# Kernel tuning notes

Measured on AMD Instinct MI355X. Metric: run time of the kernel, lower is better.

## Reference

```python
import jax, jax.numpy as jnp
from jax import lax
import numpy as np

L, B, D, H = 256, 128, 512, 512


def setup_inputs() -> dict:
    rng = np.random.default_rng(0)
    # random projective-ish dependency trees: node 0 is root, head[i] < i
    heads = np.full((B, L), -1, dtype=np.int64)
    for i in range(1, L):
        heads[:, i] = rng.integers(0, i, size=B)
    # bottom-up traversal order (children have larger index than parent)
    indexes = np.tile(np.arange(L - 1, -1, -1, dtype=np.int32)[:, None], (1, B))  # [L,B]
    # cm_full[b,p,j] = 1 if j is a child of p in tree b
    cm_full = (heads[:, None, :] == np.arange(L)[None, :, None]).astype(np.float32)  # [B,L,L]
    child_mask = cm_full[:, ::-1, :].transpose(1, 0, 2).copy()  # [L,B,L] aligned with indexes
    # top-down order: root first (ascending index works since head[i] < i)
    td_node = np.tile(np.arange(L, dtype=np.int32)[:, None], (1, B))  # [L,B]
    td_parent_idx = np.maximum(heads.T, 0).astype(np.int32)  # [L,B]
    td_parent_valid = (heads.T >= 0).astype(np.float32)  # [L,B], 0 at root
    root_index = np.zeros(B, dtype=np.int32)

    key = jax.random.key(0)
    ks = jax.random.split(key, 7)
    sx = 1.0 / np.sqrt(D)
    sh = 1.0 / np.sqrt(H)
    return {
        "emb": jax.random.normal(ks[0], (L, B, D), jnp.float32),
        "indexes": jnp.asarray(indexes),
        "child_mask": jnp.asarray(child_mask),
        "td_node": jnp.asarray(td_node),
        "td_parent_idx": jnp.asarray(td_parent_idx),
        "td_parent_valid": jnp.asarray(td_parent_valid),
        "root_index": jnp.asarray(root_index),
        "dt_Wx": jax.random.normal(ks[1], (D, 3 * H), jnp.float32) * sx,
        "dt_Uh": jax.random.normal(ks[2], (H, 3 * H), jnp.float32) * sh,
        "dt_b": jnp.zeros((3 * H,), jnp.float32),
        "td_Wx": jax.random.normal(ks[3], (D, 3 * H), jnp.float32) * sx,
        "td_Uh": jax.random.normal(ks[4], (H, 3 * H), jnp.float32) * sh,
        "td_b": jnp.zeros((3 * H,), jnp.float32),
    }


def _gru_cell(x, h, Wx, Uh, b):
    # standard GRU: gates laid out as [r, z, n]
    xg = x @ Wx + b
    hg = h @ Uh
    xr, xz, xn = jnp.split(xg, 3, axis=-1)
    hr, hz, hn = jnp.split(hg, 3, axis=-1)
    r = jax.nn.sigmoid(xr + hr)
    z = jax.nn.sigmoid(xz + hz)
    n = jnp.tanh(xn + r * hn)
    return (1.0 - z) * n + z * h


def reference(emb, indexes, child_mask, td_node, td_parent_idx, td_parent_valid,
              root_index, dt_Wx, dt_Uh, dt_b, td_Wx, td_Uh, td_b):
    Ld, Bd, Dd = emb.shape
    Hd = dt_Uh.shape[0]
    barange = jnp.arange(Bd)

    # ---- bottom-up (DT) pass: h_prev = sum of children hiddens ----
    x_dt = jnp.take_along_axis(emb, indexes[:, :, None], axis=0)  # [L,B,D]

    def dt_step(Hs, xs):
        x, node, cmask = xs                      # [B,D], [B], [B,L]
        h = jnp.einsum('bl,blh->bh', cmask, Hs)  # sum over children
        hn = _gru_cell(x, h, dt_Wx, dt_Uh, dt_b)
        return Hs.at[barange, node].set(hn), None

    Hdt, _ = lax.scan(dt_step, jnp.zeros((Bd, Ld, Hd), emb.dtype),
                      (x_dt, indexes, child_mask))

    # ---- top-down (TD) pass: h_prev = parent hidden (zeros at root) ----
    x_td = jnp.take_along_axis(emb, td_node[:, :, None], axis=0)  # [L,B,D]

    def td_step(Hs, xs):
        x, node, pidx, pvalid = xs
        h = Hs[barange, pidx] * pvalid[:, None]
        hn = _gru_cell(x, h, td_Wx, td_Uh, td_b)
        return Hs.at[barange, node].set(hn), None

    Htd, _ = lax.scan(td_step, jnp.zeros((Bd, Ld, Hd), emb.dtype),
                      (x_td, td_node, td_parent_idx, td_parent_valid))

    outputs = jnp.concatenate([Hdt, Htd], axis=-1)  # [B,L,2H] (batch-first as original)
    root_h = jnp.concatenate([Hdt[barange, root_index], Htd[barange, root_index]], axis=-1)
    output_t = root_h[None]  # [1,B,2H]
    return outputs, output_t
```

## Files before the change

### kernel.cpp

```cpp
#include <hip/hip_runtime.h>
#include <hip/hip_cooperative_groups.h>


#define NL 256
#define NB 128
#define NH 512
#define NG (NB * NL)
#define WLDS 98304

typedef short short8 __attribute__((ext_vector_type(8)));
typedef float f32x4 __attribute__((ext_vector_type(4)));

__device__ __forceinline__ float bf2f(unsigned short u) {
  union { unsigned int i; float f; } c; c.i = ((unsigned int)u) << 16; return c.f;
}
__device__ __forceinline__ unsigned short f2bf(float f) {
  union { float f; unsigned int i; } c; c.f = f;
  return (unsigned short)((c.i + 0x7FFFu + ((c.i >> 16) & 1u)) >> 16);
}
__device__ __forceinline__ short8 pk_bf16(f32x4 a, f32x4 b) {
  union { unsigned int u[4]; short8 s; } r;
  asm("v_cvt_pk_bf16_f32 %0, %1, %2" : "=v"(r.u[0]) : "v"(a[0]), "v"(a[1]));
  asm("v_cvt_pk_bf16_f32 %0, %1, %2" : "=v"(r.u[1]) : "v"(a[2]), "v"(a[3]));
  asm("v_cvt_pk_bf16_f32 %0, %1, %2" : "=v"(r.u[2]) : "v"(b[0]), "v"(b[1]));
  asm("v_cvt_pk_bf16_f32 %0, %1, %2" : "=v"(r.u[3]) : "v"(b[2]), "v"(b[3]));
  return r.s;
}
__device__ __forceinline__ void atom_pk_bf16(unsigned short* p, unsigned int ud) {
  asm volatile("global_atomic_pk_add_bf16 %0, %1, off" :: "v"((void*)p), "v"(ud) : "memory");
}

__global__ void prep_wt4(const float* __restrict__ w0, const float* __restrict__ w1,
                         const float* __restrict__ w2, const float* __restrict__ w3,
                         unsigned short* __restrict__ wt) {
  __shared__ float t[32][33];
  const float* w = blockIdx.z == 0 ? w0 : blockIdx.z == 1 ? w1 : blockIdx.z == 2 ? w2 : w3;
  unsigned short* dst = wt + (size_t)blockIdx.z * 1536 * 512;
  int n0 = blockIdx.x * 32, k0 = blockIdx.y * 32;
  int tx = threadIdx.x & 31, ty = threadIdx.x >> 5;
  #pragma unroll
  for (int i = 0; i < 4; ++i)
    t[ty + 8 * i][tx] = w[(size_t)(k0 + ty + 8 * i) * 1536 + n0 + tx];
  __syncthreads();
  #pragma unroll
  for (int i = 0; i < 4; ++i)
    dst[(size_t)(n0 + ty + 8 * i) * 512 + k0 + tx] = f2bf(t[tx][ty + 8 * i]);
}

__global__ void prep_sched(const int* __restrict__ td_pidx,
                           const float* __restrict__ td_pval,
                           int* __restrict__ sched, int* __restrict__ meta,
                           int* __restrict__ gidx, int* __restrict__ pslot) {
  __shared__ unsigned char dep[NB][NL];
  __shared__ unsigned short cnb[NB][256];
  __shared__ int cnt[256];
  __shared__ int off[257];
  __shared__ int dmax_s;
  const int tid = threadIdx.x;
  for (int j = tid; j < NB * 256; j += 256) ((unsigned short*)cnb)[j] = 0;
  if (tid == 0) dmax_s = 0;
  __syncthreads();
  if (tid < NB) {
    int b = tid, lmax = 0;
    for (int i = 0; i < NL; ++i) {
      float pv = td_pval[i * NB + b];
      int pi = td_pidx[i * NB + b];
      int d = (pv != 0.f) ? (int)dep[b][pi] + 1 : 0;
      dep[b][i] = (unsigned char)d;
      cnb[b][d]++;
      lmax = max(lmax, d);
    }
    atomicMax(&dmax_s, lmax);
  }
  __syncthreads();
  {
    int s = 0;
    for (int b = 0; b < NB; ++b) s += cnb[b][tid];
    cnt[tid] = s;
  }
  __syncthreads();
  if (tid == 0) {
    int s = 0;
    for (int d = 0; d < 256; ++d) { off[d] = s; s += cnt[d]; }
    off[256] = s;
  }
  __syncthreads();
  {
    int run = off[tid];
    for (int b = 0; b < NB; ++b) {
      int t = cnb[b][tid];
      cnb[b][tid] = (unsigned short)run;
      run += t;
    }
  }
  __syncthreads();
  if (tid < NB) {
    int b = tid;
    for (int i = 0; i < NL; ++i) {
      float pv = td_pval[i * NB + b];
      int pi = td_pidx[i * NB + b];
      int d = dep[b][i];
      int g = cnb[b][d]++;
      sched[g] = (b << 8) | i;
      gidx[b * NL + i] = g;
      pslot[g] = (pv != 0.f) ? gidx[b * NL + pi] : -1;
    }
  }
  if (tid == 0) meta[0] = dmax_s;
  __syncthreads();
  meta[1 + tid] = off[tid];
  meta[257 + tid] = cnt[tid];
}

__global__ void prep_xc(const float* __restrict__ emb, const int* __restrict__ sched,
                        unsigned short* __restrict__ Xc) {
  int g = blockIdx.x * 4 + (threadIdx.x >> 6);
  int lane = threadIdx.x & 63;
  int e = sched[g];
  int b = e >> 8, node = e & 255;
  const float* src = emb + ((size_t)node * NB + b) * 512 + lane * 8;
  f32x4 v0 = *(const f32x4*)src;
  f32x4 v1 = *(const f32x4*)(src + 4);
  *(short8*)(Xc + (size_t)g * 512 + lane * 8) = pk_bf16(v0, v1);
}

__launch_bounds__(512, 2)
__global__ void tree_gru(const float* __restrict__ dt_b,
                         const float* __restrict__ td_b,
                         const unsigned short* __restrict__ wt,
                         const unsigned short* __restrict__ Xc,
                         unsigned short* __restrict__ Hdt,
                         unsigned short* __restrict__ Htd,
                         const unsigned short* __restrict__ zrow,
                         const int* __restrict__ sched,
                         const int* __restrict__ meta,
                         const int* __restrict__ pslot,
                         const int* __restrict__ root_index,
                         float* __restrict__ out) {
  extern __shared__ unsigned char lds[];
  const int tid = threadIdx.x;
  const int bi  = blockIdx.x;
  const int pass = bi >> 7;
  const int rep  = (bi >> 5) & 3;
  const int cg   = bi & 31;
  const int w  = tid >> 6, l = tid & 63;
  const int lm = l & 15, kg = l >> 4;
  const int col = cg * 16 + lm;

  for (int idx = tid; idx < 6144; idx += 512) {
    int k8  = idx & 63;
    int n   = (idx >> 6) & 15;
    int g   = (idx >> 10) % 3;
    int mat = idx / 3072;
    const unsigned short* src = wt + (size_t)(pass * 2 + mat) * (1536 * 512)
                                   + (size_t)(g * 512 + cg * 16 + n) * 512 + k8 * 8;
    short8 v = *(const short8*)src;
    int off = ((mat * 3 + g) * 16 + n) * 1024 + ((k8 * 16) ^ ((n & 7) << 4));
    *(short8*)(lds + off) = v;
  }
  unsigned char* Xb = lds + WLDS;
  unsigned char* Hb = lds + WLDS + 16384;
  __syncthreads();

  const float* bias = pass ? td_b : dt_b;
  const float br = bias[col], bz = bias[NH + col], bn = bias[2 * NH + col];
  const int base_wr = (0 * 16 + lm) * 1024;
  const int base_wz = (1 * 16 + lm) * 1024;
  const int base_wn = (2 * 16 + lm) * 1024;
  const int base_ur = (3 * 16 + lm) * 1024;
  const int base_uz = (4 * 16 + lm) * 1024;
  const int base_un = (5 * 16 + lm) * 1024;
  const int wswz = (lm & 7) << 4;

  const int srow = tid >> 3, sslot = tid & 7;
  const int dsw = ((sslot ^ (srow & 7)) << 4);

  cooperative_groups::grid_group grid = cooperative_groups::this_grid();
  const int Dmax = meta[0];

  for (int p = 0; p <= Dmax; ++p) {
    const int d = pass ? p : (Dmax - p);
    const int off_d = meta[1 + d];
    const int cnt_d = meta[257 + d];
    const int T = (cnt_d + 127) >> 7;
    for (int t = rep; t < T; t += 4) {
      const int g0 = off_d + t * 128;
      const int rows = min(128, cnt_d - t * 128);
      const unsigned short *sx[2], *sh[2];
      #pragma unroll
      for (int i = 0; i < 2; ++i) {
        int r = min(i * 64 + srow, rows - 1);
        int gg = g0 + r;
        sx[i] = Xc + (size_t)gg * 512 + sslot * 8;
        if (pass == 0) {
          sh[i] = Hdt + (size_t)gg * 512 + sslot * 8;
        } else {
          int ps = pslot[gg];
          sh[i] = (ps >= 0 ? Htd + (size_t)ps * 512 : zrow) + sslot * 8;
        }
      }
      short8 rx0 = *(const short8*)sx[0], rx1 = *(const short8*)sx[1];
      short8 rh0 = *(const short8*)sh[0], rh1 = *(const short8*)sh[1];
      f32x4 aR = {0,0,0,0}, aZ = {0,0,0,0}, aXN = {0,0,0,0}, aHN = {0,0,0,0};
      for (int c = 0; c < 8; ++c) {
        __syncthreads();
        *(short8*)(Xb + (srow)      * 128 + dsw) = rx0;
        *(short8*)(Xb + (64 + srow) * 128 + dsw) = rx1;
        *(short8*)(Hb + (srow)      * 128 + dsw) = rh0;
        *(short8*)(Hb + (64 + srow) * 128 + dsw) = rh1;
        if (c < 7) {
          rx0 = *(const short8*)(sx[0] + (c + 1) * 64);
          rx1 = *(const short8*)(sx[1] + (c + 1) * 64);
          rh0 = *(const short8*)(sh[0] + (c + 1) * 64);
          rh1 = *(const short8*)(sh[1] + (c + 1) * 64);
        }
        __syncthreads();
        #pragma unroll
        for (int ks = 0; ks < 2; ++ks) {
          const int so = (((ks << 2) | kg) ^ (lm & 7)) << 4;
          const int arow = w * 16 + lm;
          short8 ax = *(const short8*)(Xb + arow * 128 + so);
          short8 ah = *(const short8*)(Hb + arow * 128 + so);
          const int kb = (c * 128 + ks * 64 + kg * 16) ^ wswz;
          short8 bwr = *(const short8*)(lds + base_wr + kb);
          short8 bwz = *(const short8*)(lds + base_wz + kb);
          short8 bwn = *(const short8*)(lds + base_wn + kb);
          short8 bur = *(const short8*)(lds + base_ur + kb);
          short8 buz = *(const short8*)(lds + base_uz + kb);
          short8 bun = *(const short8*)(lds + base_un + kb);
          aR  = __builtin_amdgcn_mfma_f32_16x16x32_bf16(ax, bwr, aR, 0, 0, 0);
          aZ  = __builtin_amdgcn_mfma_f32_16x16x32_bf16(ax, bwz, aZ, 0, 0, 0);
          aXN = __builtin_amdgcn_mfma_f32_16x16x32_bf16(ax, bwn, aXN, 0, 0, 0);
          aR  = __builtin_amdgcn_mfma_f32_16x16x32_bf16(ah, bur, aR, 0, 0, 0);
          aZ  = __builtin_amdgcn_mfma_f32_16x16x32_bf16(ah, buz, aZ, 0, 0, 0);
          aHN = __builtin_amdgcn_mfma_f32_16x16x32_bf16(ah, bun, aHN, 0, 0, 0);
        }
      }
      #pragma unroll
      for (int q = 0; q < 4; ++q) {
        const int r = w * 16 + kg * 4 + q;
        if (r >= rows) continue;
        const int g = g0 + r;
        const int e = sched[g];
        const int bO = e >> 8, node = e & 255;
        const int ps = pslot[g];
        float hprev;
        if (pass == 0) hprev = bf2f(Hdt[(size_t)g * 512 + col]);
        else           hprev = (ps >= 0) ? bf2f(Htd[(size_t)ps * 512 + col]) : 0.f;
        float rr = 1.f / (1.f + __expf(-(aR[q] + br)));
        float zz = 1.f / (1.f + __expf(-(aZ[q] + bz)));
        float e2 = __expf(2.f * (aXN[q] + bn + rr * aHN[q]));
        float nn = (e2 - 1.f) / (e2 + 1.f);
        float h = (1.f - zz) * nn + zz * hprev;
        __builtin_nontemporal_store(h, &out[((size_t)bO * NL + node) * 1024 + pass * 512 + col]);
        float ho = __shfl_xor(h, 1);
        if (!(lm & 1)) {
          unsigned int ud;
          asm("v_cvt_pk_bf16_f32 %0, %1, %2" : "=v"(ud) : "v"(h), "v"(ho));
          if (pass == 0) {
            if (ps >= 0) atom_pk_bf16(Hdt + (size_t)ps * 512 + col, ud);
          } else {
            *(unsigned int*)(Htd + (size_t)g * 512 + col) = ud;
          }
        }
      }
    }
    grid.sync();
  }

  if (bi < NB) {
    int b = bi, root = root_index[b];
    for (int c = tid; c < 1024; c += 512)
      out[(size_t)NB * NL * 1024 + (size_t)b * 1024 + c] =
          out[((size_t)b * NL + root) * 1024 + c];
  }
}

extern "C" void kernel_launch(void* const* d_in, const int* in_sizes, int n_in,
                              void* d_out, int out_size, void* d_ws, size_t ws_size,
                              hipStream_t stream) {
  (void)in_sizes; (void)n_in; (void)out_size; (void)ws_size;
  const float* emb      = (const float*)d_in[0];
  const int*   td_pidx  = (const int*)d_in[4];
  const float* td_pval  = (const float*)d_in[5];
  const int*   root_idx = (const int*)d_in[6];
  const float* dt_Wx    = (const float*)d_in[7];
  const float* dt_Uh    = (const float*)d_in[8];
  const float* dt_b     = (const float*)d_in[9];
  const float* td_Wx    = (const float*)d_in[10];
  const float* td_Uh    = (const float*)d_in[11];
  const float* td_b     = (const float*)d_in[12];
  float* out = (float*)d_out;

  unsigned short* wt   = (unsigned short*)d_ws;
  unsigned short* Xc   = wt + (size_t)4 * 1536 * 512;
  unsigned short* Hdt  = Xc + (size_t)NG * NH;
  unsigned short* zrow = Hdt + (size_t)NG * NH;
  unsigned short* Htd  = zrow + NH;
  int* sched = (int*)(Htd + (size_t)NG * NH);
  int* meta  = sched + NG;
  int* gidx  = meta + 520;
  int* pslot = gidx + NG;

  (void)hipMemsetAsync(Hdt, 0, ((size_t)NG * NH + NH) * 2, stream);
  prep_wt4<<<dim3(48, 16, 4), dim3(256), 0, stream>>>(dt_Wx, dt_Uh, td_Wx, td_Uh, wt);
  prep_sched<<<dim3(1), dim3(256), 0, stream>>>(td_pidx, td_pval, sched, meta, gidx, pslot);
  prep_xc<<<dim3(NG / 4), dim3(256), 0, stream>>>(emb, sched, Xc);

  (void)hipFuncSetAttribute((const void*)tree_gru,
                            hipFuncAttributeMaxDynamicSharedMemorySize, 131072);

  void* args[] = {
    (void*)&dt_b, (void*)&td_b, (void*)&wt, (void*)&Xc, (void*)&Hdt, (void*)&Htd,
    (void*)&zrow, (void*)&sched, (void*)&meta, (void*)&pslot, (void*)&root_idx, (void*)&out
  };
  (void)hipLaunchCooperativeKernel((const void*)tree_gru, dim3(256), dim3(512),
                                   args, 131072u, stream);
}
```

Baseline: 1.635 ms.

## Retile tree GRU to 256x64 tiles with 32x32 MFMA and deferred output write

The tree GRU kernel moves from 128-row by 16-column tiles with resident LDS weights to 256-row by 64-column tiles. It uses 32x32x16 MFMAs, and weights are streamed per K-chunk alongside the activations, starting at a staggered K offset per column group. The fp32 output scatter and root copy leave the recurrent loop. Hidden states are stored as bf16 in a new buffer and expanded by a separate finalize kernel, and h_prev is read back from LDS instead of global memory. The aim is more MFMA work per LDS load and less global traffic inside the serialized level loop. The cost is reloading weights from global/L2 on every tile, fewer tiles per level to spread across blocks, and an extra bf16 round trip for outputs.

```diff
diff --git a/kernel.cpp b/kernel.cpp
--- a/kernel.cpp
+++ b/kernel.cpp
@@ -6,10 +6,10 @@
 #define NB 128
 #define NH 512
 #define NG (NB * NL)
-#define WLDS 98304
 
 typedef short short8 __attribute__((ext_vector_type(8)));
 typedef float f32x4 __attribute__((ext_vector_type(4)));
+typedef float f32x16 __attribute__((ext_vector_type(16)));
 
 __device__ __forceinline__ float bf2f(unsigned short u) {
   union { unsigned int i; float f; } c; c.i = ((unsigned int)u) << 16; return c.f;
@@ -130,50 +130,44 @@
                          const unsigned short* __restrict__ wt,
                          const unsigned short* __restrict__ Xc,
                          unsigned short* __restrict__ Hdt,
+                         unsigned short* __restrict__ Hfd,
                          unsigned short* __restrict__ Htd,
                          const unsigned short* __restrict__ zrow,
-                         const int* __restrict__ sched,
                          const int* __restrict__ meta,
-                         const int* __restrict__ pslot,
-                         const int* __restrict__ root_index,
-                         float* __restrict__ out) {
+                         const int* __restrict__ pslot) {
   extern __shared__ unsigned char lds[];
+  unsigned char* Axb = lds;
+  unsigned char* Ahb = lds + 32768;
+  unsigned char* Bwb = lds + 65536;
   const int tid = threadIdx.x;
   const int bi  = blockIdx.x;
   const int pass = bi >> 7;
-  const int rep  = (bi >> 5) & 3;
-  const int cg   = bi & 31;
-  const int w  = tid >> 6, l = tid & 63;
-  const int lm = l & 15, kg = l >> 4;
-  const int col = cg * 16 + lm;
-
-  for (int idx = tid; idx < 6144; idx += 512) {
-    int k8  = idx & 63;
-    int n   = (idx >> 6) & 15;
-    int g   = (idx >> 10) % 3;
-    int mat = idx / 3072;
-    const unsigned short* src = wt + (size_t)(pass * 2 + mat) * (1536 * 512)
-                                   + (size_t)(g * 512 + cg * 16 + n) * 512 + k8 * 8;
-    short8 v = *(const short8*)src;
-    int off = ((mat * 3 + g) * 16 + n) * 1024 + ((k8 * 16) ^ ((n & 7) << 4));
-    *(short8*)(lds + off) = v;
-  }
-  unsigned char* Xb = lds + WLDS;
-  unsigned char* Hb = lds + WLDS + 16384;
-  __syncthreads();
-
+  const int rp   = (bi >> 3) & 15;
+  const int cg   = bi & 7;
+  const int w = tid >> 6, l = tid & 63;
+  const int wr = w >> 1, wc = w & 1;
+  const int l31 = l & 31, lh = l >> 5;
+  const int col = cg * 64 + wc * 32 + l31;
   const float* bias = pass ? td_b : dt_b;
   const float br = bias[col], bz = bias[NH + col], bn = bias[2 * NH + col];
-  const int base_wr = (0 * 16 + lm) * 1024;
-  const int base_wz = (1 * 16 + lm) * 1024;
-  const int base_wn = (2 * 16 + lm) * 1024;
-  const int base_ur = (3 * 16 + lm) * 1024;
-  const int base_uz = (4 * 16 + lm) * 1024;
-  const int base_un = (5 * 16 + lm) * 1024;
-  const int wswz = (lm & 7) << 4;
-
-  const int srow = tid >> 3, sslot = tid & 7;
-  const int dsw = ((sslot ^ (srow & 7)) << 4);
+
+  const unsigned short* bsrc[6];
+  int bdst[6];
+  #pragma unroll
+  for (int i = 0; i < 6; ++i) {
+    int j = tid + 512 * i;
+    int nrow = j >> 3, slot = j & 7;
+    int s = nrow >> 6, n = nrow & 63;
+    int side = (s >= 3) ? 1 : 0;
+    int gate = s - side * 3;
+    bsrc[i] = wt + (size_t)(pass * 2 + side) * (1536 * 512)
+                 + (size_t)(gate * 512 + cg * 64 + n) * 512 + slot * 8;
+    bdst[i] = nrow * 128 + ((slot * 16) ^ ((nrow & 7) << 4));
+  }
+  const int srow = tid >> 1;
+  const int sh64 = (tid & 1) * 64;
+  const int sdswz = (srow & 7) << 4;
+  const int rsw = (l31 & 7) << 4;
 
   cooperative_groups::grid_group grid = cooperative_groups::this_grid();
   const int Dmax = meta[0];
@@ -182,97 +176,153 @@
     const int d = pass ? p : (Dmax - p);
     const int off_d = meta[1 + d];
     const int cnt_d = meta[257 + d];
-    const int T = (cnt_d + 127) >> 7;
-    for (int t = rep; t < T; t += 4) {
-      const int g0 = off_d + t * 128;
-      const int rows = min(128, cnt_d - t * 128);
-      const unsigned short *sx[2], *sh[2];
-      #pragma unroll
-      for (int i = 0; i < 2; ++i) {
-        int r = min(i * 64 + srow, rows - 1);
-        int gg = g0 + r;
-        sx[i] = Xc + (size_t)gg * 512 + sslot * 8;
-        if (pass == 0) {
-          sh[i] = Hdt + (size_t)gg * 512 + sslot * 8;
-        } else {
-          int ps = pslot[gg];
-          sh[i] = (ps >= 0 ? Htd + (size_t)ps * 512 : zrow) + sslot * 8;
+    const int T = (cnt_d + 255) >> 8;
+    for (int t = rp; t < T; t += 16) {
+      const int g0 = off_d + t * 256;
+      const int rows = min(256, cnt_d - t * 256);
+      const int gg = g0 + min(srow, rows - 1);
+      const unsigned short* sxp = Xc + (size_t)gg * 512 + (tid & 1) * 32;
+      const unsigned short* shp;
+      if (pass == 0) {
+        shp = Hdt + (size_t)gg * 512 + (tid & 1) * 32;
+      } else {
+        int ps = pslot[gg];
+        shp = (ps >= 0 ? Htd + (size_t)ps * 512 : zrow) + (tid & 1) * 32;
+      }
+      short8 rx[4], rh[4], rb[6];
+      const int c0 = (cg + 1) & 7;
+      #pragma unroll
+      for (int jj = 0; jj < 4; ++jj) {
+        rx[jj] = *(const short8*)(sxp + c0 * 64 + jj * 8);
+        rh[jj] = *(const short8*)(shp + c0 * 64 + jj * 8);
+      }
+      #pragma unroll
+      for (int i = 0; i < 6; ++i) rb[i] = *(const short8*)(bsrc[i] + c0 * 64);
+
+      f32x16 aR[2], aZ[2], aXN[2], aHN[2];
+      #pragma unroll
+      for (int rf = 0; rf < 2; ++rf) {
+        #pragma unroll
+        for (int e = 0; e < 16; ++e) { aR[rf][e] = 0.f; aZ[rf][e] = 0.f; aXN[rf][e] = 0.f; aHN[rf][e] = 0.f; }
+      }
+
+      for (int ci = 0; ci < 8; ++ci) {
+        const int kb0 = ((cg + 1 + ci) & 7) * 0;
+        (void)kb0;
+        __syncthreads();
+        #pragma unroll
+        for (int jj = 0; jj < 4; ++jj) {
+          *(short8*)(Axb + srow * 128 + ((sh64 + jj * 16) ^ sdswz)) = rx[jj];
+          *(short8*)(Ahb + srow * 128 + ((sh64 + jj * 16) ^ sdswz)) = rh[jj];
         }
-      }
-      short8 rx0 = *(const short8*)sx[0], rx1 = *(const short8*)sx[1];
-      short8 rh0 = *(const short8*)sh[0], rh1 = *(const short8*)sh[1];
-      f32x4 aR = {0,0,0,0}, aZ = {0,0,0,0}, aXN = {0,0,0,0}, aHN = {0,0,0,0};
-      for (int c = 0; c < 8; ++c) {
-        __syncthreads();
-        *(short8*)(Xb + (srow)      * 128 + dsw) = rx0;
-        *(short8*)(Xb + (64 + srow) * 128 + dsw) = rx1;
-        *(short8*)(Hb + (srow)      * 128 + dsw) = rh0;
-        *(short8*)(Hb + (64 + srow) * 128 + dsw) = rh1;
-        if (c < 7) {
-          rx0 = *(const short8*)(sx[0] + (c + 1) * 64);
-          rx1 = *(const short8*)(sx[1] + (c + 1) * 64);
-          rh0 = *(const short8*)(sh[0] + (c + 1) * 64);
-          rh1 = *(const short8*)(sh[1] + (c + 1) * 64);
+        #pragma unroll
+        for (int i = 0; i < 6; ++i) *(short8*)(Bwb + bdst[i]) = rb[i];
+        if (ci < 7) {
+          const int cn = (cg + 2 + ci) & 7;
+          #pragma unroll
+          for (int jj = 0; jj < 4; ++jj) {
+            rx[jj] = *(const short8*)(sxp + cn * 64 + jj * 8);
+            rh[jj] = *(const short8*)(shp + cn * 64 + jj * 8);
+          }
+          #pragma unroll
+          for (int i = 0; i < 6; ++i) rb[i] = *(const short8*)(bsrc[i] + cn * 64);
         }
         __syncthreads();
         #pragma unroll
-        for (int ks = 0; ks < 2; ++ks) {
-          const int so = (((ks << 2) | kg) ^ (lm & 7)) << 4;
-          const int arow = w * 16 + lm;
-          short8 ax = *(const short8*)(Xb + arow * 128 + so);
-          short8 ah = *(const short8*)(Hb + arow * 128 + so);
-          const int kb = (c * 128 + ks * 64 + kg * 16) ^ wswz;
-          short8 bwr = *(const short8*)(lds + base_wr + kb);
-          short8 bwz = *(const short8*)(lds + base_wz + kb);
-          short8 bwn = *(const short8*)(lds + base_wn + kb);
-          short8 bur = *(const short8*)(lds + base_ur + kb);
-          short8 buz = *(const short8*)(lds + base_uz + kb);
-          short8 bun = *(const short8*)(lds + base_un + kb);
-          aR  = __builtin_amdgcn_mfma_f32_16x16x32_bf16(ax, bwr, aR, 0, 0, 0);
-          aZ  = __builtin_amdgcn_mfma_f32_16x16x32_bf16(ax, bwz, aZ, 0, 0, 0);
-          aXN = __builtin_amdgcn_mfma_f32_16x16x32_bf16(ax, bwn, aXN, 0, 0, 0);
-          aR  = __builtin_amdgcn_mfma_f32_16x16x32_bf16(ah, bur, aR, 0, 0, 0);
-          aZ  = __builtin_amdgcn_mfma_f32_16x16x32_bf16(ah, buz, aZ, 0, 0, 0);
-          aHN = __builtin_amdgcn_mfma_f32_16x16x32_bf16(ah, bun, aHN, 0, 0, 0);
+        for (int ks = 0; ks < 4; ++ks) {
+          const int kb = (ks * 32 + lh * 16) ^ rsw;
+          short8 ax0 = *(const short8*)(Axb + (wr * 64 + l31) * 128 + kb);
+          short8 ax1 = *(const short8*)(Axb + (wr * 64 + 32 + l31) * 128 + kb);
+          short8 ah0 = *(const short8*)(Ahb + (wr * 64 + l31) * 128 + kb);
+          short8 ah1 = *(const short8*)(Ahb + (wr * 64 + 32 + l31) * 128 + kb);
+          short8 b0 = *(const short8*)(Bwb + (0 * 64 + wc * 32 + l31) * 128 + kb);
+          short8 b1 = *(const short8*)(Bwb + (1 * 64 + wc * 32 + l31) * 128 + kb);
+          short8 b2 = *(const short8*)(Bwb + (2 * 64 + wc * 32 + l31) * 128 + kb);
+          short8 b3 = *(const short8*)(Bwb + (3 * 64 + wc * 32 + l31) * 128 + kb);
+          short8 b4 = *(const short8*)(Bwb + (4 * 64 + wc * 32 + l31) * 128 + kb);
+          short8 b5 = *(const short8*)(Bwb + (5 * 64 + wc * 32 + l31) * 128 + kb);
+          aR[0]  = __builtin_amdgcn_mfma_f32_32x32x16_bf16(ax0, b0, aR[0], 0, 0, 0);
+          aR[1]  = __builtin_amdgcn_mfma_f32_32x32x16_bf16(ax1, b0, aR[1], 0, 0, 0);
+          aZ[0]  = __builtin_amdgcn_mfma_f32_32x32x16_bf16(ax0, b1, aZ[0], 0, 0, 0);
+          aZ[1]  = __builtin_amdgcn_mfma_f32_32x32x16_bf16(ax1, b1, aZ[1], 0, 0, 0);
+          aXN[0] = __builtin_amdgcn_mfma_f32_32x32x16_bf16(ax0, b2, aXN[0], 0, 0, 0);
+          aXN[1] = __builtin_amdgcn_mfma_f32_32x32x16_bf16(ax1, b2, aXN[1], 0, 0, 0);
+          aR[0]  = __builtin_amdgcn_mfma_f32_32x32x16_bf16(ah0, b3, aR[0], 0, 0, 0);
+          aR[1]  = __builtin_amdgcn_mfma_f32_32x32x16_bf16(ah1, b3, aR[1], 0, 0, 0);
+          aZ[0]  = __builtin_amdgcn_mfma_f32_32x32x16_bf16(ah0, b4, aZ[0], 0, 0, 0);
+          aZ[1]  = __builtin_amdgcn_mfma_f32_32x32x16_bf16(ah1, b4, aZ[1], 0, 0, 0);
+          aHN[0] = __builtin_amdgcn_mfma_f32_32x32x16_bf16(ah0, b5, aHN[0], 0, 0, 0);
+          aHN[1] = __builtin_amdgcn_mfma_f32_32x32x16_bf16(ah1, b5, aHN[1], 0, 0, 0);
         }
       }
       #pragma unroll
-      for (int q = 0; q < 4; ++q) {
-        const int r = w * 16 + kg * 4 + q;
-        if (r >= rows) continue;
-        const int g = g0 + r;
-        const int e = sched[g];
-        const int bO = e >> 8, node = e & 255;
-        const int ps = pslot[g];
-        float hprev;
-        if (pass == 0) hprev = bf2f(Hdt[(size_t)g * 512 + col]);
-        else           hprev = (ps >= 0) ? bf2f(Htd[(size_t)ps * 512 + col]) : 0.f;
-        float rr = 1.f / (1.f + __expf(-(aR[q] + br)));
-        float zz = 1.f / (1.f + __expf(-(aZ[q] + bz)));
-        float e2 = __expf(2.f * (aXN[q] + bn + rr * aHN[q]));
-        float nn = (e2 - 1.f) / (e2 + 1.f);
-        float h = (1.f - zz) * nn + zz * hprev;
-        __builtin_nontemporal_store(h, &out[((size_t)bO * NL + node) * 1024 + pass * 512 + col]);
-        float ho = __shfl_xor(h, 1);
-        if (!(lm & 1)) {
-          unsigned int ud;
-          asm("v_cvt_pk_bf16_f32 %0, %1, %2" : "=v"(ud) : "v"(h), "v"(ho));
-          if (pass == 0) {
-            if (ps >= 0) atom_pk_bf16(Hdt + (size_t)ps * 512 + col, ud);
-          } else {
-            *(unsigned int*)(Htd + (size_t)g * 512 + col) = ud;
+      for (int rf = 0; rf < 2; ++rf) {
+        #pragma unroll
+        for (int reg = 0; reg < 16; ++reg) {
+          const int row = wr * 64 + rf * 32 + (reg & 3) + 8 * (reg >> 2) + 4 * lh;
+          if (row < rows) {
+            const int g = g0 + row;
+            const int hb = row * 128 + ((2 * (wc * 32 + l31)) ^ ((row & 7) << 4));
+            const float hprev = bf2f(*(const unsigned short*)(Ahb + hb));
+            float rr = 1.f / (1.f + __expf(-(aR[rf][reg] + br)));
+            float zz = 1.f / (1.f + __expf(-(aZ[rf][reg] + bz)));
+            float e2 = __expf(2.f * (aXN[rf][reg] + bn + rr * aHN[rf][reg]));
+            float nn = (e2 - 1.f) / (e2 + 1.f);
+            float h = (1.f - zz) * nn + zz * hprev;
+            float ho = __shfl_xor(h, 1);
+            if (!(l & 1)) {
+              unsigned int ud;
+              asm("v_cvt_pk_bf16_f32 %0, %1, %2" : "=v"(ud) : "v"(h), "v"(ho));
+              if (pass == 0) {
+                *(unsigned int*)(Hfd + (size_t)g * 512 + col) = ud;
+                int ps = pslot[g];
+                if (ps >= 0) atom_pk_bf16(Hdt + (size_t)ps * 512 + col, ud);
+              } else {
+                *(unsigned int*)(Htd + (size_t)g * 512 + col) = ud;
+              }
+            }
           }
         }
       }
     }
     grid.sync();
   }
-
-  if (bi < NB) {
-    int b = bi, root = root_index[b];
-    for (int c = tid; c < 1024; c += 512)
-      out[(size_t)NB * NL * 1024 + (size_t)b * 1024 + c] =
-          out[((size_t)b * NL + root) * 1024 + c];
+}
+
+__global__ void finalize(const unsigned short* __restrict__ Hfd,
+                         const unsigned short* __restrict__ Htd,
+                         const int* __restrict__ sched,
+                         const int* __restrict__ root_index,
+                         float* __restrict__ out) {
+  const int g = blockIdx.x * 16 + (threadIdx.x >> 4);
+  const int part = threadIdx.x & 15;
+  const int e = sched[g];
+  const int b = e >> 8, node = e & 255;
+  float* dst = out + ((size_t)b * NL + node) * 1024;
+  const bool isroot = (node == root_index[b]);
+  float* dst2 = out + (size_t)NB * NL * 1024 + (size_t)b * 1024;
+  const unsigned short* s1 = Hfd + (size_t)g * 512 + part * 32;
+  const unsigned short* s2 = Htd + (size_t)g * 512 + part * 32;
+  #pragma unroll
+  for (int half = 0; half < 2; ++half) {
+    const unsigned short* s = half ? s2 : s1;
+    const int o = half * 512 + part * 32;
+    #pragma unroll
+    for (int j = 0; j < 4; ++j) {
+      short8 v = *(const short8*)(s + j * 8);
+      f32x4 lo, hi;
+      #pragma unroll
+      for (int q = 0; q < 4; ++q) {
+        lo[q] = bf2f((unsigned short)v[q]);
+        hi[q] = bf2f((unsigned short)v[4 + q]);
+      }
+      __builtin_nontemporal_store(lo, (f32x4*)(dst + o + j * 8));
+      __builtin_nontemporal_store(hi, (f32x4*)(dst + o + j * 8 + 4));
+      if (isroot) {
+        *(f32x4*)(dst2 + o + j * 8) = lo;
+        *(f32x4*)(dst2 + o + j * 8 + 4) = hi;
+      }
+    }
   }
 }
 
@@ -296,7 +346,8 @@
   unsigned short* Xc   = wt + (size_t)4 * 1536 * 512;
   unsigned short* Hdt  = Xc + (size_t)NG * NH;
   unsigned short* zrow = Hdt + (size_t)NG * NH;
-  unsigned short* Htd  = zrow + NH;
+  unsigned short* Hfd  = zrow + NH;
+  unsigned short* Htd  = Hfd + (size_t)NG * NH;
   int* sched = (int*)(Htd + (size_t)NG * NH);
   int* meta  = sched + NG;
   int* gidx  = meta + 520;
@@ -308,12 +359,13 @@
   prep_xc<<<dim3(NG / 4), dim3(256), 0, stream>>>(emb, sched, Xc);
 
   (void)hipFuncSetAttribute((const void*)tree_gru,
-                            hipFuncAttributeMaxDynamicSharedMemorySize, 131072);
+                            hipFuncAttributeMaxDynamicSharedMemorySize, 114688);
 
   void* args[] = {
-    (void*)&dt_b, (void*)&td_b, (void*)&wt, (void*)&Xc, (void*)&Hdt, (void*)&Htd,
-    (void*)&zrow, (void*)&sched, (void*)&meta, (void*)&pslot, (void*)&root_idx, (void*)&out
+    (void*)&dt_b, (void*)&td_b, (void*)&wt, (void*)&Xc, (void*)&Hdt, (void*)&Hfd,
+    (void*)&Htd, (void*)&zrow, (void*)&meta, (void*)&pslot
   };
   (void)hipLaunchCooperativeKernel((const void*)tree_gru, dim3(256), dim3(512),
-                                   args, 131072u, stream);
-}
+                                   args, 114688u, stream);
+  finalize<<<dim3(NG / 16), dim3(256), 0, stream>>>(Hfd, Htd, sched, root_idx, out);
+}
```

After: 2.561 ms. 1.57x slower.

## Replace grid-wide barriers with per-level dependency counters and deferred output writes

Applied to the files above, without the earlier changes.

Swaps the cooperative grid.sync after every depth level for per-level atomic completion counters. Each block spin-waits only on the level it depends on, and blocks with no tiles at a level skip it, so the DT and TD passes can proceed independently. Final hidden states are now kept in bf16 workspace (a new Hfd buffer for DT) and expanded to fp32 output in one coalesced epilogue that also writes the root rows. hprev is read from the LDS tile instead of global memory, the K-chunk start is staggered per column group, and the block-to-work mapping is changed. The cost is spin-wait polling, extra atomics and fences, an extra workspace buffer, and a larger memset.

```diff
diff --git a/kernel.cpp b/kernel.cpp
--- a/kernel.cpp
+++ b/kernel.cpp
@@ -1,12 +1,10 @@
 #include <hip/hip_runtime.h>
-#include <hip/hip_cooperative_groups.h>
 
 
 #define NL 256
 #define NB 128
 #define NH 512
 #define NG (NB * NL)
-#define WLDS 98304
 
 typedef short short8 __attribute__((ext_vector_type(8)));
 typedef float f32x4 __attribute__((ext_vector_type(4)));
@@ -28,6 +26,15 @@
 }
 __device__ __forceinline__ void atom_pk_bf16(unsigned short* p, unsigned int ud) {
   asm volatile("global_atomic_pk_add_bf16 %0, %1, off" :: "v"((void*)p), "v"(ud) : "memory");
+}
+
+__device__ __forceinline__ void level_wait(unsigned int* c, unsigned int target) {
+  if (threadIdx.x == 0) {
+    while (__hip_atomic_load(c, __ATOMIC_RELAXED, __HIP_MEMORY_SCOPE_AGENT) < target)
+      __builtin_amdgcn_s_sleep(8);
+  }
+  __syncthreads();
+  __builtin_amdgcn_fence(__ATOMIC_ACQUIRE, "agent");
 }
 
 __global__ void prep_wt4(const float* __restrict__ w0, const float* __restrict__ w1,
@@ -131,18 +138,20 @@
                          const unsigned short* __restrict__ Xc,
                          unsigned short* __restrict__ Hdt,
                          unsigned short* __restrict__ Htd,
+                         unsigned short* __restrict__ Hfd,
                          const unsigned short* __restrict__ zrow,
-                         const int* __restrict__ sched,
                          const int* __restrict__ meta,
                          const int* __restrict__ pslot,
+                         unsigned int* __restrict__ ctr,
+                         const int* __restrict__ sched,
                          const int* __restrict__ root_index,
                          float* __restrict__ out) {
   extern __shared__ unsigned char lds[];
   const int tid = threadIdx.x;
   const int bi  = blockIdx.x;
-  const int pass = bi >> 7;
-  const int rep  = (bi >> 5) & 3;
-  const int cg   = bi & 31;
+  const int cg   = bi >> 3;
+  const int pass = (bi >> 2) & 1;
+  const int rep  = bi & 3;
   const int w  = tid >> 6, l = tid & 63;
   const int lm = l & 15, kg = l >> 4;
   const int col = cg * 16 + lm;
@@ -158,8 +167,8 @@
     int off = ((mat * 3 + g) * 16 + n) * 1024 + ((k8 * 16) ^ ((n & 7) << 4));
     *(short8*)(lds + off) = v;
   }
-  unsigned char* Xb = lds + WLDS;
-  unsigned char* Hb = lds + WLDS + 16384;
+  unsigned char* Xb = lds + 98304;
+  unsigned char* Hb = lds + 98304 + 16384;
   __syncthreads();
 
   const float* bias = pass ? td_b : dt_b;
@@ -171,18 +180,22 @@
   const int base_uz = (4 * 16 + lm) * 1024;
   const int base_un = (5 * 16 + lm) * 1024;
   const int wswz = (lm & 7) << 4;
-
   const int srow = tid >> 3, sslot = tid & 7;
   const int dsw = ((sslot ^ (srow & 7)) << 4);
-
-  cooperative_groups::grid_group grid = cooperative_groups::this_grid();
+  const int ck = cg >> 2;
+  const int ccol2 = 2 * ((cg & 3) * 16 + lm);
   const int Dmax = meta[0];
+  unsigned int* doneP = ctr + pass * 256;
 
   for (int p = 0; p <= Dmax; ++p) {
     const int d = pass ? p : (Dmax - p);
     const int off_d = meta[1 + d];
     const int cnt_d = meta[257 + d];
     const int T = (cnt_d + 127) >> 7;
+    if (T <= rep) continue;
+    const int dl = pass ? d - 1 : d + 1;
+    if (dl >= 0 && dl <= Dmax)
+      level_wait(doneP + dl, (unsigned int)meta[257 + dl] * 32u);
     for (int t = rep; t < T; t += 4) {
       const int g0 = off_d + t * 128;
       const int rows = min(128, cnt_d - t * 128);
@@ -199,20 +212,26 @@
           sh[i] = (ps >= 0 ? Htd + (size_t)ps * 512 : zrow) + sslot * 8;
         }
       }
-      short8 rx0 = *(const short8*)sx[0], rx1 = *(const short8*)sx[1];
-      short8 rh0 = *(const short8*)sh[0], rh1 = *(const short8*)sh[1];
+      const int c0 = (ck + 1) & 7;
+      short8 rx0 = *(const short8*)(sx[0] + c0 * 64);
+      short8 rx1 = *(const short8*)(sx[1] + c0 * 64);
+      short8 rh0 = *(const short8*)(sh[0] + c0 * 64);
+      short8 rh1 = *(const short8*)(sh[1] + c0 * 64);
       f32x4 aR = {0,0,0,0}, aZ = {0,0,0,0}, aXN = {0,0,0,0}, aHN = {0,0,0,0};
-      for (int c = 0; c < 8; ++c) {
+      #pragma unroll
+      for (int ci = 0; ci < 8; ++ci) {
+        const int c = (ck + 1 + ci) & 7;
         __syncthreads();
         *(short8*)(Xb + (srow)      * 128 + dsw) = rx0;
         *(short8*)(Xb + (64 + srow) * 128 + dsw) = rx1;
         *(short8*)(Hb + (srow)      * 128 + dsw) = rh0;
         *(short8*)(Hb + (64 + srow) * 128 + dsw) = rh1;
-        if (c < 7) {
-          rx0 = *(const short8*)(sx[0] + (c + 1) * 64);
-          rx1 = *(const short8*)(sx[1] + (c + 1) * 64);
-          rh0 = *(const short8*)(sh[0] + (c + 1) * 64);
-          rh1 = *(const short8*)(sh[1] + (c + 1) * 64);
+        if (ci < 7) {
+          const int cn = (ck + 2 + ci) & 7;
+          rx0 = *(const short8*)(sx[0] + cn * 64);
+          rx1 = *(const short8*)(sx[1] + cn * 64);
+          rh0 = *(const short8*)(sh[0] + cn * 64);
+          rh1 = *(const short8*)(sh[1] + cn * 64);
         }
         __syncthreads();
         #pragma unroll
@@ -241,38 +260,71 @@
         const int r = w * 16 + kg * 4 + q;
         if (r >= rows) continue;
         const int g = g0 + r;
-        const int e = sched[g];
-        const int bO = e >> 8, node = e & 255;
-        const int ps = pslot[g];
-        float hprev;
-        if (pass == 0) hprev = bf2f(Hdt[(size_t)g * 512 + col]);
-        else           hprev = (ps >= 0) ? bf2f(Htd[(size_t)ps * 512 + col]) : 0.f;
+        const float hprev = bf2f(*(const unsigned short*)(
+            Hb + r * 128 + (ccol2 ^ ((r & 7) << 4))));
         float rr = 1.f / (1.f + __expf(-(aR[q] + br)));
         float zz = 1.f / (1.f + __expf(-(aZ[q] + bz)));
         float e2 = __expf(2.f * (aXN[q] + bn + rr * aHN[q]));
         float nn = (e2 - 1.f) / (e2 + 1.f);
         float h = (1.f - zz) * nn + zz * hprev;
-        __builtin_nontemporal_store(h, &out[((size_t)bO * NL + node) * 1024 + pass * 512 + col]);
         float ho = __shfl_xor(h, 1);
         if (!(lm & 1)) {
           unsigned int ud;
           asm("v_cvt_pk_bf16_f32 %0, %1, %2" : "=v"(ud) : "v"(h), "v"(ho));
           if (pass == 0) {
+            atom_pk_bf16(Hfd + (size_t)g * 512 + col, ud);
+            int ps = pslot[g];
             if (ps >= 0) atom_pk_bf16(Hdt + (size_t)ps * 512 + col, ud);
           } else {
-            *(unsigned int*)(Htd + (size_t)g * 512 + col) = ud;
+            atom_pk_bf16(Htd + (size_t)g * 512 + col, ud);
           }
         }
       }
-    }
-    grid.sync();
-  }
-
-  if (bi < NB) {
-    int b = bi, root = root_index[b];
-    for (int c = tid; c < 1024; c += 512)
-      out[(size_t)NB * NL * 1024 + (size_t)b * 1024 + c] =
-          out[((size_t)b * NL + root) * 1024 + c];
+      asm volatile("s_waitcnt vmcnt(0)" ::: "memory");
+      __syncthreads();
+      if (tid == 0) {
+        __hip_atomic_fetch_add(doneP + d, (unsigned int)rows,
+                               __ATOMIC_RELAXED, __HIP_MEMORY_SCOPE_AGENT);
+        __hip_atomic_fetch_add(ctr + 512 + pass, (unsigned int)rows,
+                               __ATOMIC_RELAXED, __HIP_MEMORY_SCOPE_AGENT);
+      }
+    }
+  }
+
+  level_wait(ctr + 512, (unsigned int)NG * 32u);
+  level_wait(ctr + 513, (unsigned int)NG * 32u);
+  #pragma unroll
+  for (int it = 0; it < 4; ++it) {
+    const int g = bi * 128 + it * 32 + (tid >> 4);
+    const int part = tid & 15;
+    const int e = sched[g];
+    const int b = e >> 8, node = e & 255;
+    float* dst = out + ((size_t)b * NL + node) * 1024;
+    const bool isroot = (node == root_index[b]);
+    float* dst2 = out + (size_t)NB * NL * 1024 + (size_t)b * 1024;
+    const unsigned short* s1 = Hfd + (size_t)g * 512 + part * 32;
+    const unsigned short* s2 = Htd + (size_t)g * 512 + part * 32;
+    #pragma unroll
+    for (int half = 0; half < 2; ++half) {
+      const unsigned short* s = half ? s2 : s1;
+      const int o = half * 512 + part * 32;
+      #pragma unroll
+      for (int j = 0; j < 4; ++j) {
+        short8 v = *(const short8*)(s + j * 8);
+        f32x4 lo, hi;
+        #pragma unroll
+        for (int q = 0; q < 4; ++q) {
+          lo[q] = bf2f((unsigned short)v[q]);
+          hi[q] = bf2f((unsigned short)v[4 + q]);
+        }
+        __builtin_nontemporal_store(lo, (f32x4*)(dst + o + j * 8));
+        __builtin_nontemporal_store(hi, (f32x4*)(dst + o + j * 8 + 4));
+        if (isroot) {
+          *(f32x4*)(dst2 + o + j * 8) = lo;
+          *(f32x4*)(dst2 + o + j * 8 + 4) = hi;
+        }
+      }
+    }
   }
 }
 
@@ -295,14 +347,17 @@
   unsigned short* wt   = (unsigned short*)d_ws;
   unsigned short* Xc   = wt + (size_t)4 * 1536 * 512;
   unsigned short* Hdt  = Xc + (size_t)NG * NH;
-  unsigned short* zrow = Hdt + (size_t)NG * NH;
-  unsigned short* Htd  = zrow + NH;
-  int* sched = (int*)(Htd + (size_t)NG * NH);
+  unsigned short* Htd  = Hdt + (size_t)NG * NH;
+  unsigned short* Hfd  = Htd + (size_t)NG * NH;
+  unsigned short* zrow = Hfd + (size_t)NG * NH;
+  unsigned int*   ctr  = (unsigned int*)(zrow + NH);
+  int* sched = (int*)(ctr + 520);
   int* meta  = sched + NG;
   int* gidx  = meta + 520;
   int* pslot = gidx + NG;
 
-  (void)hipMemsetAsync(Hdt, 0, ((size_t)NG * NH + NH) * 2, stream);
+  const size_t zbytes = (size_t)3 * NG * NH * 2 + NH * 2 + 520 * 4;
+  (void)hipMemsetAsync(Hdt, 0, zbytes, stream);
   prep_wt4<<<dim3(48, 16, 4), dim3(256), 0, stream>>>(dt_Wx, dt_Uh, td_Wx, td_Uh, wt);
   prep_sched<<<dim3(1), dim3(256), 0, stream>>>(td_pidx, td_pval, sched, meta, gidx, pslot);
   prep_xc<<<dim3(NG / 4), dim3(256), 0, stream>>>(emb, sched, Xc);
@@ -312,7 +367,8 @@
 
   void* args[] = {
     (void*)&dt_b, (void*)&td_b, (void*)&wt, (void*)&Xc, (void*)&Hdt, (void*)&Htd,
-    (void*)&zrow, (void*)&sched, (void*)&meta, (void*)&pslot, (void*)&root_idx, (void*)&out
+    (void*)&Hfd, (void*)&zrow, (void*)&meta, (void*)&pslot, (void*)&ctr,
+    (void*)&sched, (void*)&root_idx, (void*)&out
   };
   (void)hipLaunchCooperativeKernel((const void*)tree_gru, dim3(256), dim3(512),
                                    args, 131072u, stream);
```

New measurement: 1.659 ms. About the same (+1.5%).
